# Performance work log

Hardware: AMD Instinct MI355X
Metric: run time of the kernel (lower is better)

## Reference

```python
import jax, jax.numpy as jnp
import numpy as np

ENT_TYPES = 9
INNER_DIM = 64
BIG_NEG = 1e12


def _rope_tables(seq_len, dim, dtype):
    # sinusoidal_position_embedding: interleaved [sin, cos] of pos * 10000^(-2i/d)
    pos = jnp.arange(seq_len, dtype=jnp.float32)[:, None]            # [S,1]
    inv_freq = jnp.power(10000.0, -2.0 * jnp.arange(dim // 2, dtype=jnp.float32) / dim)
    ang = pos * inv_freq                                             # [S,D/2]
    emb = jnp.stack([jnp.sin(ang), jnp.cos(ang)], axis=-1).reshape(seq_len, dim)  # [S,D]
    cos_pos = jnp.repeat(emb[:, 1::2], 2, axis=-1).astype(dtype)     # [S,D]
    sin_pos = jnp.repeat(emb[:, ::2], 2, axis=-1).astype(dtype)      # [S,D]
    return cos_pos, sin_pos


def _rotate_half(x):
    # stack([-x[...,1::2], x[...,::2]], -1).reshape(x.shape)
    return jnp.stack([-x[..., 1::2], x[..., ::2]], axis=-1).reshape(x.shape)


def setup_inputs() -> dict:
    key = jax.random.key(0)
    k1, k2 = jax.random.split(key)
    B, S, H = 16, 512, 1024
    last_hidden_state = jax.random.normal(k1, (B, S, H), dtype=jnp.float32)
    padding_mask = jnp.ones((B, S), dtype=jnp.float32)
    W = jax.random.normal(k2, (H, ENT_TYPES * INNER_DIM * 2), dtype=jnp.float32) * (1.0 / np.sqrt(H))
    b = jnp.zeros((ENT_TYPES * INNER_DIM * 2,), dtype=jnp.float32)
    return {"last_hidden_state": last_hidden_state, "padding_mask": padding_mask, "W": W, "b": b}


def reference(last_hidden_state, padding_mask, W, b):
    B, S, _ = last_hidden_state.shape
    H, D = ENT_TYPES, INNER_DIM
    out = last_hidden_state @ W + b                 # [B,S,H*2D]
    out = out.reshape(B, S, H, 2 * D)
    qw, kw = out[..., :D], out[..., D:]             # [B,S,H,D]

    cos_pos, sin_pos = _rope_tables(S, D, qw.dtype)  # [S,D]
    cos_pos = cos_pos[None, :, None, :]
    sin_pos = sin_pos[None, :, None, :]
    qw = qw * cos_pos + _rotate_half(qw) * sin_pos
    kw = kw * cos_pos + _rotate_half(kw) * sin_pos

    logits = jnp.einsum('bmhd,bnhd->bhmn', qw, kw)   # [B,H,S,S]
    pad = padding_mask[:, None, None, :]             # mask over key dim
    logits = logits * pad - (1.0 - pad) * BIG_NEG
    tril = jnp.tril(jnp.ones((S, S), dtype=logits.dtype), -1)
    logits = logits - tril * BIG_NEG
    return logits / jnp.sqrt(jnp.asarray(D, dtype=logits.dtype))
```

## Files before the change

kernel.cpp:

```cpp
#include <hip/hip_runtime.h>

#define EN 9
#define DD 64
#define SS 512
#define HH 1024
#define NOUT 1152

typedef float f32x4 __attribute__((ext_vector_type(4)));

#define GPTR(p) ((const __attribute__((address_space(1))) void*)(p))
#define LPTR(p) ((__attribute__((address_space(3))) void*)(p))

__device__ inline unsigned short f2bf(float f) {
  unsigned int u = __float_as_uint(f);
  return (unsigned short)((u + 0x7FFFu + ((u >> 16) & 1u)) >> 16);
}

__device__ inline int pk4_fp8(float a, float b, float c, float d) {
  int v = __builtin_amdgcn_cvt_pk_fp8_f32(a, b, 0, false);
  v = __builtin_amdgcn_cvt_pk_fp8_f32(c, d, v, true);
  return v;
}

__global__ __launch_bounds__(256) void prep_kernel(
    const float* __restrict__ W, const float* __restrict__ X,
    unsigned char* __restrict__ Wf8, unsigned char* __restrict__ Xf8,
    float* __restrict__ ctab, float* __restrict__ stab) {
  if (blockIdx.x < 288u) {
    __shared__ float t[64][65];
    const int k0 = (blockIdx.x / 18) * 64;
    const int n0 = (blockIdx.x % 18) * 64;
    const int r = threadIdx.x >> 6;
    const int c = threadIdx.x & 63;
#pragma unroll
    for (int i = 0; i < 16; ++i) {
      const int kk = (i << 2) + r;
      t[kk][c] = W[(size_t)(k0 + kk) * NOUT + n0 + c];
    }
    __syncthreads();
#pragma unroll
    for (int i = 0; i < 2; ++i) {
      const int p = (i << 8) + threadIdx.x;
      const int n = p >> 3, cc = p & 7;
      const int kk = cc << 3;
      const int lo = pk4_fp8(t[kk][n], t[kk + 1][n], t[kk + 2][n], t[kk + 3][n]);
      const int hi =
          pk4_fp8(t[kk + 4][n], t[kk + 5][n], t[kk + 6][n], t[kk + 7][n]);
      const int gn = n0 + n;
      int2 v;
      v.x = lo;
      v.y = hi;
      *(int2*)(Wf8 + (size_t)gn * HH + k0 + ((cc ^ (gn & 7)) << 3)) = v;
    }
  } else if (blockIdx.x < 304u) {
    const int bt = blockIdx.x - 288;
#pragma unroll
    for (int j = 0; j < 4; ++j) {
      const int id = bt * 1024 + j * 256 + threadIdx.x;
      const int s = id >> 5, i = id & 31;
      const float freq = expf(-(float)(2 * i) * (9.210340371976184f / 64.0f));
      const float ang = (float)s * freq;
      ctab[id] = cosf(ang);
      stab[id] = sinf(ang);
    }
  } else {
    const int bt = blockIdx.x - 304;
#pragma unroll
    for (int j = 0; j < 4; ++j) {
      const int C = bt * 1024 + (j << 8) + threadIdx.x;
      const int row = C >> 7, c = C & 127;
      const float4 v0 = *(const float4*)(X + (size_t)C * 8);
      const float4 v1 = *(const float4*)(X + (size_t)C * 8 + 4);
      int2 v;
      v.x = pk4_fp8(v0.x, v0.y, v0.z, v0.w);
      v.y = pk4_fp8(v1.x, v1.y, v1.z, v1.w);
      *(int2*)(Xf8 + (size_t)row * HH + ((c >> 3) << 6) +
               (((c ^ row) & 7) << 3)) = v;
    }
  }
}

__global__ __launch_bounds__(256, 4) void proj_rope_kernel(
    const unsigned char* __restrict__ Xf8, const unsigned char* __restrict__ Wf8,
    const float* __restrict__ bias, const float* __restrict__ ctab,
    const float* __restrict__ stab, unsigned short* __restrict__ QK) {
  __shared__ __align__(16) unsigned char sm[32768];
  const int tid = threadIdx.x;
  const int lane = tid & 63;
  const int wid = tid >> 6;
  const int wr = wid >> 1, wc = wid & 1;
  const int f = blockIdx.x;
  const int wkr = (f & 7) * 72 + (f >> 3);
  const int m0 = (wkr / 9) << 7;
  const int n0 = (wkr % 9) << 7;

  f32x4 acc[4][4];
#pragma unroll
  for (int i = 0; i < 4; ++i)
#pragma unroll
    for (int j = 0; j < 4; ++j) acc[i][j] = (f32x4){0.f, 0.f, 0.f, 0.f};

#define STAGE(BUF, KT)                                                       \
  {                                                                          \
    const int kt_ = (KT);                                                    \
    unsigned char* dst_ = sm + (BUF)*16384;                                  \
    _Pragma("unroll") for (int it = 0; it < 2; ++it) {                       \
      const int u_ = (it << 8) + tid;                                        \
      const int r_ = u_ >> 2, g_ = u_ & 3;                                   \
      __builtin_amdgcn_global_load_lds(                                      \
          GPTR(Xf8 + (size_t)(m0 + r_) * HH + kt_ + (g_ << 4)),              \
          LPTR(dst_ + (((it << 8) + (wid << 6)) << 4)), 16, 0, 0);           \
      __builtin_amdgcn_global_load_lds(                                      \
          GPTR(Wf8 + (size_t)(n0 + r_) * HH + kt_ + (g_ << 4)),              \
          LPTR(dst_ + 8192 + (((it << 8) + (wid << 6)) << 4)), 16, 0, 0);    \
    }                                                                        \
  }

#define COMPUTE(BUF)                                                         \
  {                                                                          \
    const unsigned char* smc_ = sm + (BUF)*16384;                            \
    __builtin_amdgcn_s_setprio(1);                                           \
    _Pragma("unroll") for (int kb = 0; kb < 2; ++kb) {                       \
      long aL[4], bL[4];                                                     \
      const int c8 = (kb << 2) + (lane >> 4);                                \
      _Pragma("unroll") for (int i = 0; i < 4; ++i) {                        \
        const int ra = (wr << 6) + (i << 4) + (lane & 15);                   \
        aL[i] = *(const long*)(smc_ + (ra << 6) + (((c8 ^ ra) & 7) << 3));   \
        const int rb = (wc << 6) + (i << 4) + (lane & 15);                   \
        bL[i] = *(const long*)(smc_ + 8192 + (rb << 6) +                     \
                               (((c8 ^ rb) & 7) << 3));                      \
      }                                                                      \
      _Pragma("unroll") for (int mi = 0; mi < 4; ++mi)                       \
          _Pragma("unroll") for (int ni = 0; ni < 4; ++ni) acc[mi][ni] =     \
          __builtin_amdgcn_mfma_f32_16x16x32_fp8_fp8(aL[mi], bL[ni],         \
                                                     acc[mi][ni], 0, 0, 0);  \
    }                                                                        \
    __builtin_amdgcn_s_setprio(0);                                           \
  }

  STAGE(0, 0)
#pragma unroll 1
  for (int t = 0; t < 15; ++t) {
    STAGE((t + 1) & 1, (t + 1) << 6)
    asm volatile("s_waitcnt vmcnt(4)" ::: "memory");
    __builtin_amdgcn_s_barrier();
    __builtin_amdgcn_sched_barrier(0);
    COMPUTE(t & 1)
    __builtin_amdgcn_sched_barrier(0);
    __builtin_amdgcn_s_barrier();
  }
  asm volatile("s_waitcnt vmcnt(0)" ::: "memory");
  __builtin_amdgcn_s_barrier();
  __builtin_amdgcn_sched_barrier(0);
  COMPUTE(1)

#pragma unroll
  for (int mi = 0; mi < 4; ++mi) {
#pragma unroll
    for (int ni = 0; ni < 4; ++ni) {
      const int n = n0 + (wc << 6) + (ni << 4) + (lane & 15);
      const float bn = bias[n];
      const int h = n >> 7, t = (n >> 6) & 1, d = n & 63;
      const int i2 = d >> 1;
      const bool ev = (d & 1) == 0;
#pragma unroll
      for (int r = 0; r < 4; ++r) {
        const int m = m0 + (wr << 6) + (mi << 4) + ((lane >> 4) << 2) + r;
        const int s = m & (SS - 1);
        const int bb = m >> 9;
        const float v = acc[mi][ni][r] + bn;
        const float p = __shfl_xor(v, 1);
        const float cs = ctab[(s << 5) + i2];
        const float sn = stab[(s << 5) + i2];
        const float o = ev ? (v * cs - p * sn) : (v * cs + p * sn);
        QK[((((size_t)bb * EN + h) * 2 + t) * SS + s) * DD + d] = f2bf(o);
      }
    }
  }
}

__global__ __launch_bounds__(256, 4) void logits_kernel(
    const unsigned short* __restrict__ QK, const float* __restrict__ pmask,
    float* __restrict__ out) {
  __shared__ __align__(16) unsigned char sm[32768];
  const int tid = threadIdx.x;
  const int lane = tid & 63;
  const int wid = tid >> 6;
  const int wr = wid >> 1, wc = wid & 1;
  const int f = blockIdx.x;
  const int wkr = (f & 7) * 288 + (f >> 3);
  const int bh = wkr >> 4;
  const int bb = bh / EN;
  const int tm = (wkr >> 2) & 3, tn = wkr & 3;
  const int mq0 = tm << 7, nk0 = tn << 7;
  const unsigned short* Qb = QK + (size_t)bh * 2 * SS * DD;
  const unsigned short* Kb = Qb + SS * DD;

#pragma unroll
  for (int it = 0; it < 4; ++it) {
    const int q = it * 256 + tid;
    const int r = q >> 3, cl = q & 7;
    const int cs = cl ^ (r & 7);
    __builtin_amdgcn_global_load_lds(
        GPTR(Qb + (size_t)(mq0 + r) * DD + (cs << 3)),
        LPTR(sm + ((it * 256 + wid * 64) << 4)), 16, 0, 0);
    __builtin_amdgcn_global_load_lds(
        GPTR(Kb + (size_t)(nk0 + r) * DD + (cs << 3)),
        LPTR(sm + 16384 + ((it * 256 + wid * 64) << 4)), 16, 0, 0);
  }
  __syncthreads();

  f32x4 acc[4][4];
#pragma unroll
  for (int i = 0; i < 4; ++i)
#pragma unroll
    for (int j = 0; j < 4; ++j) acc[i][j] = (f32x4){0.f, 0.f, 0.f, 0.f};

  typedef short bf16x8 __attribute__((ext_vector_type(8)));
#pragma unroll
  for (int kb = 0; kb < 2; ++kb) {
    bf16x8 af[4], bfr[4];
    const int ca = (kb << 2) + (lane >> 4);
#pragma unroll
    for (int i = 0; i < 4; ++i) {
      const int ra = (wr << 6) + (i << 4) + (lane & 15);
      af[i] = *(const bf16x8*)(sm + (ra << 7) + ((ca ^ (ra & 7)) << 4));
      const int rb = (wc << 6) + (i << 4) + (lane & 15);
      bfr[i] =
          *(const bf16x8*)(sm + 16384 + (rb << 7) + ((ca ^ (rb & 7)) << 4));
    }
#pragma unroll
    for (int mi = 0; mi < 4; ++mi)
#pragma unroll
      for (int ni = 0; ni < 4; ++ni)
        acc[mi][ni] = __builtin_amdgcn_mfma_f32_16x16x32_bf16(
            af[mi], bfr[ni], acc[mi][ni], 0, 0, 0);
  }

#pragma unroll
  for (int mi = 0; mi < 4; ++mi) {
#pragma unroll
    for (int ni = 0; ni < 4; ++ni) {
      const int n = nk0 + (wc << 6) + (ni << 4) + (lane & 15);
      const float pd = pmask[bb * SS + n];
      const float sub = (1.0f - pd) * 1e12f;
#pragma unroll
      for (int r = 0; r < 4; ++r) {
        const int m = mq0 + (wr << 6) + (mi << 4) + ((lane >> 4) << 2) + r;
        float v = acc[mi][ni][r] * pd - sub;
        if (m > n) v -= 1e12f;
        out[((size_t)bh * SS + m) * SS + n] = v * 0.125f;
      }
    }
  }
}

extern "C" void kernel_launch(void* const* d_in, const int* in_sizes, int n_in,
                              void* d_out, int out_size, void* d_ws,
                              size_t ws_size, hipStream_t stream) {
  const float* X = (const float*)d_in[0];
  const float* pm = (const float*)d_in[1];
  const float* W = (const float*)d_in[2];
  const float* bias = (const float*)d_in[3];
  float* out = (float*)d_out;
  unsigned char* ws = (unsigned char*)d_ws;
  unsigned short* QK = (unsigned short*)ws;
  unsigned char* Wf8 = ws + 18874368;
  float* ctab = (float*)(ws + 20054016);
  float* stab = (float*)(ws + 20119552);
  unsigned char* Xf8 = ws + 20185088;

  prep_kernel<<<dim3(1328), dim3(256), 0, stream>>>(W, X, Wf8, Xf8, ctab, stab);
  proj_rope_kernel<<<dim3(576), dim3(256), 0, stream>>>(Xf8, Wf8, bias, ctab,
                                                        stab, QK);
  logits_kernel<<<dim3(2304), dim3(256), 0, stream>>>(QK, pm, out);
}
```

Measured before the change: 62.95 us.

## Triple-buffer projection K-loop and stage epilogue through LDS for vector stores

Moves the projection GEMM from double to triple buffering in shared memory (48KB, occupancy hint lowered from 4 to 3 blocks) so two loads stay in flight ahead of compute. The RoPE epilogue now writes accumulators to an LDS scratch tile, then each thread reads 8 contiguous columns, applies bias and rotation with vectorized table loads, and issues 16-byte bf16 stores. This replaces scattered 2-byte stores and shuffles. The cost is lower occupancy and extra barriers in the epilogue.

New measurement: 63.19 us. No clear change (+0.4%).

```diff
diff --git a/kernel.cpp b/kernel.cpp
--- a/kernel.cpp
+++ b/kernel.cpp
@@ -7,6 +7,7 @@
 #define NOUT 1152
 
 typedef float f32x4 __attribute__((ext_vector_type(4)));
+typedef short short8v __attribute__((ext_vector_type(8)));
 
 #define GPTR(p) ((const __attribute__((address_space(1))) void*)(p))
 #define LPTR(p) ((__attribute__((address_space(3))) void*)(p))
@@ -80,11 +81,11 @@
   }
 }
 
-__global__ __launch_bounds__(256, 4) void proj_rope_kernel(
+__global__ __launch_bounds__(256, 3) void proj_rope_kernel(
     const unsigned char* __restrict__ Xf8, const unsigned char* __restrict__ Wf8,
     const float* __restrict__ bias, const float* __restrict__ ctab,
     const float* __restrict__ stab, unsigned short* __restrict__ QK) {
-  __shared__ __align__(16) unsigned char sm[32768];
+  __shared__ __align__(16) unsigned char sm[49152];
   const int tid = threadIdx.x;
   const int lane = tid & 63;
   const int wid = tid >> 6;
@@ -139,43 +140,77 @@
   }
 
   STAGE(0, 0)
+  STAGE(1, 64)
 #pragma unroll 1
-  for (int t = 0; t < 15; ++t) {
-    STAGE((t + 1) & 1, (t + 1) << 6)
-    asm volatile("s_waitcnt vmcnt(4)" ::: "memory");
+  for (int t = 0; t < 14; ++t) {
+    STAGE((t + 2) % 3, (t + 2) << 6)
+    asm volatile("s_waitcnt vmcnt(8)" ::: "memory");
     __builtin_amdgcn_s_barrier();
     __builtin_amdgcn_sched_barrier(0);
-    COMPUTE(t & 1)
+    COMPUTE(t % 3)
     __builtin_amdgcn_sched_barrier(0);
     __builtin_amdgcn_s_barrier();
   }
+  asm volatile("s_waitcnt vmcnt(4)" ::: "memory");
+  __builtin_amdgcn_s_barrier();
+  __builtin_amdgcn_sched_barrier(0);
+  COMPUTE(2)
+  __builtin_amdgcn_sched_barrier(0);
+  __builtin_amdgcn_s_barrier();
   asm volatile("s_waitcnt vmcnt(0)" ::: "memory");
   __builtin_amdgcn_s_barrier();
   __builtin_amdgcn_sched_barrier(0);
-  COMPUTE(1)
-
+  COMPUTE(0)
+
+  __syncthreads();
+  float* scr = (float*)sm;
+  const int erow = tid >> 3;
+  const int ec8 = (tid & 7) << 1;
 #pragma unroll
   for (int mi = 0; mi < 4; ++mi) {
 #pragma unroll
     for (int ni = 0; ni < 4; ++ni) {
-      const int n = n0 + (wc << 6) + (ni << 4) + (lane & 15);
-      const float bn = bias[n];
-      const int h = n >> 7, t = (n >> 6) & 1, d = n & 63;
-      const int i2 = d >> 1;
-      const bool ev = (d & 1) == 0;
+      const int col = (wc << 6) + (ni << 4) + (lane & 15);
 #pragma unroll
       for (int r = 0; r < 4; ++r) {
-        const int m = m0 + (wr << 6) + (mi << 4) + ((lane >> 4) << 2) + r;
-        const int s = m & (SS - 1);
-        const int bb = m >> 9;
-        const float v = acc[mi][ni][r] + bn;
-        const float p = __shfl_xor(v, 1);
-        const float cs = ctab[(s << 5) + i2];
-        const float sn = stab[(s << 5) + i2];
-        const float o = ev ? (v * cs - p * sn) : (v * cs + p * sn);
-        QK[((((size_t)bb * EN + h) * 2 + t) * SS + s) * DD + d] = f2bf(o);
+        const int row = (wr << 4) + ((lane >> 4) << 2) + r;
+        scr[row * 132 + col] = acc[mi][ni][r];
       }
     }
+    __syncthreads();
+    const int m = m0 + ((erow >> 4) << 6) + (mi << 4) + (erow & 15);
+    const int s = m & (SS - 1);
+    const int bb = m >> 9;
+#pragma unroll
+    for (int sl = 0; sl < 2; ++sl) {
+      const int c8 = ec8 + sl;
+      const int ncol = c8 << 3;
+      const int n = n0 + ncol;
+      const int h = n >> 7;
+      const int t = (n >> 6) & 1;
+      const int d0 = n & 63;
+      const float4 va = *(const float4*)&scr[erow * 132 + ncol];
+      const float4 vb = *(const float4*)&scr[erow * 132 + ncol + 4];
+      const float4 bia = *(const float4*)&bias[n];
+      const float4 bib = *(const float4*)&bias[n + 4];
+      const float4 cs = *(const float4*)&ctab[(s << 5) + (d0 >> 1)];
+      const float4 sn = *(const float4*)&stab[(s << 5) + (d0 >> 1)];
+      const float e0 = va.x + bia.x, o0 = va.y + bia.y;
+      const float e1 = va.z + bia.z, o1 = va.w + bia.w;
+      const float e2 = vb.x + bib.x, o2 = vb.y + bib.y;
+      const float e3 = vb.z + bib.z, o3 = vb.w + bib.w;
+      short8v ov;
+      ov[0] = (short)f2bf(e0 * cs.x - o0 * sn.x);
+      ov[1] = (short)f2bf(o0 * cs.x + e0 * sn.x);
+      ov[2] = (short)f2bf(e1 * cs.y - o1 * sn.y);
+      ov[3] = (short)f2bf(o1 * cs.y + e1 * sn.y);
+      ov[4] = (short)f2bf(e2 * cs.z - o2 * sn.z);
+      ov[5] = (short)f2bf(o2 * cs.z + e2 * sn.z);
+      ov[6] = (short)f2bf(e3 * cs.w - o3 * sn.w);
+      ov[7] = (short)f2bf(o3 * cs.w + e3 * sn.w);
+      *(short8v*)&QK[(((size_t)(bb * EN + h) * 2 + t) * SS + s) * DD + d0] = ov;
+    }
+    __syncthreads();
   }
 }
 
```
